# Optimization experiments

Measured on AMD Instinct MI355X. Metric: run time of the kernel, lower is better.

Reference implementation:

```python
import jax, jax.numpy as jnp
import numpy as np

INTRA_K = 16
OUTER_K = 16
MAX_PAIR = 1024


def _mahalanobis(x, cov_inv, mean):
    # x: (..., D) difference vectors; returns squared Mahalanobis-style form (...,)
    xc = x - mean
    return jnp.einsum('...i,ij,...j->...', xc, cov_inv, xc)


def setup_inputs() -> dict:
    key = jax.random.key(0)
    k1, k2, k3 = jax.random.split(key, 3)
    B, N, M = 4, 1024, 1024
    outputs = jax.random.normal(k1, (B, N, 9), dtype=jnp.float32)
    targets = jax.random.normal(k2, (B, M, 9), dtype=jnp.float32)
    mask = jax.random.randint(k3, (B, M), 0, 2).astype(bool)
    return {"outputs": outputs, "targets": targets, "mask": mask}


def reference(outputs, targets, mask):
    y_pred = outputs[:, :MAX_PAIR]                      # (B, N, 9)
    m = mask.astype(y_pred.dtype)                       # (B, M)
    cnt = m.sum()

    # mean / covariance over masked true grasps (equivalent to boolean-gather)
    mean = (targets * m[..., None]).sum((0, 1)) / cnt   # (9,)
    centered = (targets - mean) * m[..., None]          # masked rows contribute 0
    flat = centered.reshape(-1, 9)
    cov = flat.T @ flat / (cnt - 1.0)                   # (9, 9)
    cov_inv = jnp.linalg.pinv(cov)

    # intra loss: true-vs-pred pairwise distances, masked rows excluded
    diff = targets[:, :, None, :] - y_pred[:, None, :, :]   # (B, M, N, 9)
    d = _mahalanobis(diff, cov_inv, mean)                   # (B, M, N)
    neg_topk, _ = jax.lax.top_k(-d, INTRA_K)                # k smallest
    row_sum = (-neg_topk).sum(-1)                           # (B, M)
    intra_loss = (row_sum * m).sum() / cnt                  # mean over masked rows

    # outer loss: pred-vs-pred pairwise distances, no mask
    diff_r = y_pred[:, None, :, :] - y_pred[:, :, None, :]  # (B, N, N, 9); [b,i,j] = pred[b,j]-pred[b,i]
    d_r = _mahalanobis(diff_r, cov_inv, mean)               # (B, N, N)
    neg_tk, _ = jax.lax.top_k(-d_r, OUTER_K)
    outer_loss = (-neg_tk).mean()

    return intra_loss, intra_loss, outer_loss
```

## Files before the change

### kernel.cpp

```cpp
#include <hip/hip_runtime.h>
#include <math.h>

#define BB   4
#define MM   1024
#define NN   1024
#define DD   9
#define KSEL 16
#define NROW (BB * MM)
#define NSLOT (2 * NROW)
#define NBLK (NSLOT / 4)

struct Ws {
  float yT[BB * DD * NN];
  float qy[BB * NN];
  float rowsum[NSLOT];
  float part[16][55];
  float cnt;
  float mean[DD];
  float cinv[DD * DD];
};

__global__ __launch_bounds__(256) void stats_kernel(
    const float* __restrict__ targets, const int* __restrict__ mask,
    Ws* __restrict__ ws) {
  const int tid = threadIdx.x;
  const int r = blockIdx.x * 256 + tid;

  float acc[55];
#pragma unroll
  for (int k = 0; k < 55; ++k) acc[k] = 0.f;
  if (mask[r] != 0) {
    float t[DD];
#pragma unroll
    for (int k = 0; k < DD; ++k) t[k] = targets[r * DD + k];
    acc[0] = 1.f;
#pragma unroll
    for (int k = 0; k < DD; ++k) acc[1 + k] = t[k];
    int u = 10;
#pragma unroll
    for (int p = 0; p < DD; ++p)
#pragma unroll
      for (int q = p; q < DD; ++q) acc[u++] = t[p] * t[q];
  }

  __shared__ float lds[4][55];
#pragma unroll
  for (int k = 0; k < 55; ++k) {
    float v = acc[k];
#pragma unroll
    for (int off = 32; off > 0; off >>= 1) v += __shfl_down(v, off, 64);
    if ((tid & 63) == 0) lds[tid >> 6][k] = v;
  }
  __syncthreads();
  if (tid < 55)
    ws->part[blockIdx.x][tid] =
        lds[0][tid] + lds[1][tid] + lds[2][tid] + lds[3][tid];
}

__global__ __launch_bounds__(256) void prep_kernel(
    const float* __restrict__ outputs, Ws* __restrict__ ws) {
  const int tid = threadIdx.x;
  __shared__ double Sd[55];
  __shared__ float Cs[DD * DD];

  if (tid < 55) {
    double s = 0.0;
#pragma unroll
    for (int b = 0; b < 16; ++b) s += (double)ws->part[b][tid];
    Sd[tid] = s;
  }
  __syncthreads();

  if (tid < 64) {
    const int lane = tid;
    const double cnt = Sd[0];
    const int p = (lane < DD) ? lane : 0;
    double row[2 * DD];
    {
      const double mu_p = Sd[1 + p] / cnt;
#pragma unroll
      for (int q = 0; q < DD; ++q) {
        const int pp = (p < q) ? p : q;
        const int qq = (p < q) ? q : p;
        const int idx = 10 + 9 * pp - (pp * (pp - 1)) / 2 + (qq - pp);
        row[q] = (Sd[idx] - cnt * mu_p * (Sd[1 + q] / cnt)) / (cnt - 1.0);
        row[DD + q] = (p == q) ? 1.0 : 0.0;
      }
    }
#pragma unroll
    for (int c = 0; c < DD; ++c) {
      const double diag = __shfl(row[c], c, 64);
      const double dinv = 1.0 / diag;
      if (lane == c) {
#pragma unroll
        for (int q = 0; q < 2 * DD; ++q) row[q] *= dinv;
      }
      const double f = (lane == c) ? 0.0 : row[c];
#pragma unroll
      for (int q = 0; q < 2 * DD; ++q) {
        const double pv = __shfl(row[q], c, 64);
        row[q] -= f * pv;
      }
    }
    if (lane < DD) {
#pragma unroll
      for (int q = 0; q < DD; ++q) {
        const float cf = (float)row[DD + q];
        Cs[lane * DD + q] = cf;
        if (blockIdx.x == 0) ws->cinv[lane * DD + q] = cf;
      }
    }
    if (lane == 0 && blockIdx.x == 0) {
      ws->cnt = (float)cnt;
#pragma unroll
      for (int q = 0; q < DD; ++q) ws->mean[q] = (float)(Sd[1 + q] / cnt);
    }
  }
  __syncthreads();

  const int j = blockIdx.x * 256 + tid;
  const int b = j >> 10;
  const int jj = j & (NN - 1);
  float C[DD * DD];
#pragma unroll
  for (int k = 0; k < DD * DD; ++k) C[k] = Cs[k];
  float y[DD];
#pragma unroll
  for (int k = 0; k < DD; ++k) y[k] = outputs[j * DD + k];
  float q = 0.f;
#pragma unroll
  for (int p = 0; p < DD; ++p) {
    float s = 0.f;
#pragma unroll
    for (int t = 0; t < DD; ++t) s += C[p * DD + t] * y[t];
    q += y[p] * s;
    ws->yT[(b * DD + p) * NN + jj] = y[p];
  }
  ws->qy[j] = q;
}

__global__ __launch_bounds__(256) void dist_kernel(
    const float* __restrict__ outputs, const float* __restrict__ targets,
    const int* __restrict__ mask, Ws* __restrict__ ws) {
  const int wv = threadIdx.x >> 6;
  const int lane = threadIdx.x & 63;
  const int s = blockIdx.x * 4 + wv;
  const bool is_intra = (s < NROW);
  const int r = s & (NROW - 1);
  const int b = r >> 10;

  if (is_intra && mask[r] == 0) {
    if (lane == 0) ws->rowsum[s] = 0.f;
    return;
  }

  float a[DD];
  if (is_intra) {
#pragma unroll
    for (int k = 0; k < DD; ++k) a[k] = targets[r * DD + k] - ws->mean[k];
  } else {
#pragma unroll
    for (int k = 0; k < DD; ++k) a[k] = outputs[r * DD + k] + ws->mean[k];
  }
  float w[DD];
  float qa = 0.f;
#pragma unroll
  for (int p = 0; p < DD; ++p) {
    float acc = 0.f;
#pragma unroll
    for (int t = 0; t < DD; ++t) acc += ws->cinv[p * DD + t] * a[t];
    w[p] = acc;
    qa += a[p] * acc;
  }

  float v[16];
#pragma unroll
  for (int k = 0; k < 16; ++k) v[k] = 0.f;
  const float* __restrict__ yTb = ws->yT + (size_t)b * DD * NN;
#pragma unroll
  for (int p = 0; p < DD; ++p) {
    const float4* __restrict__ pl = (const float4*)(yTb + (size_t)p * NN);
#pragma unroll
    for (int c = 0; c < 4; ++c) {
      const float4 y4 = pl[c * 64 + lane];
      v[c * 4 + 0] += w[p] * y4.x;
      v[c * 4 + 1] += w[p] * y4.y;
      v[c * 4 + 2] += w[p] * y4.z;
      v[c * 4 + 3] += w[p] * y4.w;
    }
  }
  {
    const float4* __restrict__ q4 = (const float4*)(ws->qy + (size_t)b * NN);
#pragma unroll
    for (int c = 0; c < 4; ++c) {
      const float4 qv = q4[c * 64 + lane];
      v[c * 4 + 0] = qa + qv.x - 2.f * v[c * 4 + 0];
      v[c * 4 + 1] = qa + qv.y - 2.f * v[c * 4 + 1];
      v[c * 4 + 2] = qa + qv.z - 2.f * v[c * 4 + 2];
      v[c * 4 + 3] = qa + qv.w - 2.f * v[c * 4 + 3];
    }
  }

#pragma unroll
  for (int k = 2; k <= 16; k <<= 1) {
#pragma unroll
    for (int j = k >> 1; j > 0; j >>= 1) {
#pragma unroll
      for (int i = 0; i < 16; ++i) {
        const int l = i ^ j;
        if (l > i) {
          const bool up = ((i & k) == 0);
          const float lo = fminf(v[i], v[l]);
          const float hi = fmaxf(v[i], v[l]);
          v[i] = up ? lo : hi;
          v[l] = up ? hi : lo;
        }
      }
    }
  }

#pragma unroll
  for (int off = 1; off < 64; off <<= 1) {
    float pr[16];
#pragma unroll
    for (int i = 0; i < 16; ++i) pr[i] = __shfl_xor(v[i], off, 64);
#pragma unroll
    for (int i = 0; i < 16; ++i) v[i] = fminf(v[i], pr[15 - i]);
    if (off < 32) {
#pragma unroll
      for (int j = 8; j > 0; j >>= 1) {
#pragma unroll
        for (int i = 0; i < 16; ++i) {
          const int l = i ^ j;
          if (l > i) {
            const float lo = fminf(v[i], v[l]);
            const float hi = fmaxf(v[i], v[l]);
            v[i] = lo;
            v[l] = hi;
          }
        }
      }
    }
  }

  float total = v[0];
#pragma unroll
  for (int k = 1; k < 16; ++k) total += v[k];
  if (lane == 0) ws->rowsum[s] = total;
}

__global__ __launch_bounds__(256) void finalize_kernel(
    const Ws* __restrict__ ws, float* __restrict__ out) {
  const int tid = threadIdx.x;
  double li = 0.0, lo = 0.0;
  for (int k = tid; k < NROW; k += 256) {
    li += (double)ws->rowsum[k];
    lo += (double)ws->rowsum[NROW + k];
  }
#pragma unroll
  for (int off = 32; off > 0; off >>= 1) {
    li += __shfl_down(li, off, 64);
    lo += __shfl_down(lo, off, 64);
  }
  __shared__ double lds_i[4], lds_o[4];
  if ((tid & 63) == 0) {
    lds_i[tid >> 6] = li;
    lds_o[tid >> 6] = lo;
  }
  __syncthreads();
  if (tid == 0) {
    const double si = lds_i[0] + lds_i[1] + lds_i[2] + lds_i[3];
    const double so = lds_o[0] + lds_o[1] + lds_o[2] + lds_o[3];
    const float intra = (float)(si / (double)ws->cnt);
    const float outer = (float)(so / (double)(NROW * KSEL));
    out[0] = intra;
    out[1] = intra;
    out[2] = outer;
  }
}

extern "C" void kernel_launch(void* const* d_in, const int* in_sizes, int n_in,
                              void* d_out, int out_size, void* d_ws,
                              size_t ws_size, hipStream_t stream) {
  const float* outputs = (const float*)d_in[0];
  const float* targets = (const float*)d_in[1];
  const int* mask = (const int*)d_in[2];
  Ws* ws = (Ws*)d_ws;
  float* out = (float*)d_out;

  stats_kernel<<<NROW / 256, 256, 0, stream>>>(targets, mask, ws);
  prep_kernel<<<(BB * NN) / 256, 256, 0, stream>>>(outputs, ws);
  dist_kernel<<<NBLK, 256, 0, stream>>>(outputs, targets, mask, ws);
  finalize_kernel<<<1, 256, 0, stream>>>(ws, out);
}
```

Before: 97.61 us.

## Fuse stats/prep into one block and merge intra/outer rows with last-block finalize

Stats and prep are merged into a single 512-thread block, with each thread handling 8 rows and vectorized stores. The intra and outer rows for the same index now share one wave, so each yT load feeds both accumulations. Finalization runs in the last block to arrive, chosen by an atomic ticket, which removes two kernel launches. The costs are a serial single-block setup phase and more registers per wave in the distance kernel.

```diff
diff --git a/kernel.cpp b/kernel.cpp
--- a/kernel.cpp
+++ b/kernel.cpp
@@ -8,65 +8,66 @@
 #define KSEL 16
 #define NROW (BB * MM)
 #define NSLOT (2 * NROW)
-#define NBLK (NSLOT / 4)
 
 struct Ws {
   float yT[BB * DD * NN];
   float qy[BB * NN];
   float rowsum[NSLOT];
-  float part[16][55];
   float cnt;
   float mean[DD];
   float cinv[DD * DD];
+  unsigned int ticket;
 };
 
-__global__ __launch_bounds__(256) void stats_kernel(
-    const float* __restrict__ targets, const int* __restrict__ mask,
-    Ws* __restrict__ ws) {
+__global__ __launch_bounds__(512) void setup_kernel(
+    const float* __restrict__ outputs, const float* __restrict__ targets,
+    const int* __restrict__ mask, Ws* __restrict__ ws) {
   const int tid = threadIdx.x;
-  const int r = blockIdx.x * 256 + tid;
+  __shared__ float part[8][55];
+  __shared__ double Sd[55];
+  __shared__ float Cs[DD * DD];
 
   float acc[55];
 #pragma unroll
   for (int k = 0; k < 55; ++k) acc[k] = 0.f;
-  if (mask[r] != 0) {
-    float t[DD];
-#pragma unroll
-    for (int k = 0; k < DD; ++k) t[k] = targets[r * DD + k];
-    acc[0] = 1.f;
-#pragma unroll
-    for (int k = 0; k < DD; ++k) acc[1 + k] = t[k];
-    int u = 10;
-#pragma unroll
-    for (int p = 0; p < DD; ++p)
-#pragma unroll
-      for (int q = p; q < DD; ++q) acc[u++] = t[p] * t[q];
-  }
-
-  __shared__ float lds[4][55];
+  {
+    const float4* tp = (const float4*)targets + 18 * tid;
+    float4 st4[18];
+#pragma unroll
+    for (int i = 0; i < 18; ++i) st4[i] = tp[i];
+    const float* f = (const float*)st4;
+    const int4 m0 = ((const int4*)mask)[2 * tid];
+    const int4 m1 = ((const int4*)mask)[2 * tid + 1];
+    const int mk[8] = {m0.x, m0.y, m0.z, m0.w, m1.x, m1.y, m1.z, m1.w};
+#pragma unroll
+    for (int rr = 0; rr < 8; ++rr) {
+      if (mk[rr] != 0) {
+        const float* t = f + rr * DD;
+        acc[0] += 1.f;
+#pragma unroll
+        for (int k = 0; k < DD; ++k) acc[1 + k] += t[k];
+        int u = 10;
+#pragma unroll
+        for (int p = 0; p < DD; ++p)
+#pragma unroll
+          for (int q = p; q < DD; ++q) acc[u++] += t[p] * t[q];
+      }
+    }
+  }
 #pragma unroll
   for (int k = 0; k < 55; ++k) {
     float v = acc[k];
 #pragma unroll
     for (int off = 32; off > 0; off >>= 1) v += __shfl_down(v, off, 64);
-    if ((tid & 63) == 0) lds[tid >> 6][k] = v;
-  }
-  __syncthreads();
-  if (tid < 55)
-    ws->part[blockIdx.x][tid] =
-        lds[0][tid] + lds[1][tid] + lds[2][tid] + lds[3][tid];
-}
-
-__global__ __launch_bounds__(256) void prep_kernel(
-    const float* __restrict__ outputs, Ws* __restrict__ ws) {
-  const int tid = threadIdx.x;
-  __shared__ double Sd[55];
-  __shared__ float Cs[DD * DD];
+    if ((tid & 63) == 0) part[tid >> 6][k] = v;
+  }
+  if (tid == 0) ws->ticket = 0u;
+  __syncthreads();
 
   if (tid < 55) {
     double s = 0.0;
 #pragma unroll
-    for (int b = 0; b < 16; ++b) s += (double)ws->part[b][tid];
+    for (int w = 0; w < 8; ++w) s += (double)part[w][tid];
     Sd[tid] = s;
   }
   __syncthreads();
@@ -107,10 +108,10 @@
       for (int q = 0; q < DD; ++q) {
         const float cf = (float)row[DD + q];
         Cs[lane * DD + q] = cf;
-        if (blockIdx.x == 0) ws->cinv[lane * DD + q] = cf;
-      }
-    }
-    if (lane == 0 && blockIdx.x == 0) {
+        ws->cinv[lane * DD + q] = cf;
+      }
+    }
+    if (lane == 0) {
       ws->cnt = (float)cnt;
 #pragma unroll
       for (int q = 0; q < DD; ++q) ws->mean[q] = (float)(Sd[1 + q] / cnt);
@@ -118,89 +119,50 @@
   }
   __syncthreads();
 
-  const int j = blockIdx.x * 256 + tid;
-  const int b = j >> 10;
-  const int jj = j & (NN - 1);
-  float C[DD * DD];
-#pragma unroll
-  for (int k = 0; k < DD * DD; ++k) C[k] = Cs[k];
-  float y[DD];
-#pragma unroll
-  for (int k = 0; k < DD; ++k) y[k] = outputs[j * DD + k];
-  float q = 0.f;
-#pragma unroll
-  for (int p = 0; p < DD; ++p) {
-    float s = 0.f;
-#pragma unroll
-    for (int t = 0; t < DD; ++t) s += C[p * DD + t] * y[t];
-    q += y[p] * s;
-    ws->yT[(b * DD + p) * NN + jj] = y[p];
-  }
-  ws->qy[j] = q;
+  {
+    const int j0 = tid * 8;
+    const int b = j0 >> 10;
+    const int jj = j0 & (NN - 1);
+    float C[DD * DD];
+#pragma unroll
+    for (int k = 0; k < DD * DD; ++k) C[k] = Cs[k];
+    const float4* op4 = (const float4*)outputs + 18 * tid;
+    float4 so4[18];
+#pragma unroll
+    for (int i = 0; i < 18; ++i) so4[i] = op4[i];
+    const float* f = (const float*)so4;
+#pragma unroll
+    for (int g = 0; g < 2; ++g) {
+      float qv[4];
+#pragma unroll
+      for (int rr = 0; rr < 4; ++rr) {
+        const float* y = f + (g * 4 + rr) * DD;
+        float qq = 0.f;
+#pragma unroll
+        for (int p = 0; p < DD; ++p) {
+          float s = 0.f;
+#pragma unroll
+          for (int t = 0; t < DD; ++t) s += C[p * DD + t] * y[t];
+          qq += y[p] * s;
+        }
+        qv[rr] = qq;
+      }
+#pragma unroll
+      for (int p = 0; p < DD; ++p) {
+        float4 o;
+        o.x = f[(g * 4 + 0) * DD + p];
+        o.y = f[(g * 4 + 1) * DD + p];
+        o.z = f[(g * 4 + 2) * DD + p];
+        o.w = f[(g * 4 + 3) * DD + p];
+        *(float4*)(&ws->yT[(b * DD + p) * NN + jj + g * 4]) = o;
+      }
+      *(float4*)(&ws->qy[b * NN + jj + g * 4]) =
+          make_float4(qv[0], qv[1], qv[2], qv[3]);
+    }
+  }
 }
 
-__global__ __launch_bounds__(256) void dist_kernel(
-    const float* __restrict__ outputs, const float* __restrict__ targets,
-    const int* __restrict__ mask, Ws* __restrict__ ws) {
-  const int wv = threadIdx.x >> 6;
-  const int lane = threadIdx.x & 63;
-  const int s = blockIdx.x * 4 + wv;
-  const bool is_intra = (s < NROW);
-  const int r = s & (NROW - 1);
-  const int b = r >> 10;
-
-  if (is_intra && mask[r] == 0) {
-    if (lane == 0) ws->rowsum[s] = 0.f;
-    return;
-  }
-
-  float a[DD];
-  if (is_intra) {
-#pragma unroll
-    for (int k = 0; k < DD; ++k) a[k] = targets[r * DD + k] - ws->mean[k];
-  } else {
-#pragma unroll
-    for (int k = 0; k < DD; ++k) a[k] = outputs[r * DD + k] + ws->mean[k];
-  }
-  float w[DD];
-  float qa = 0.f;
-#pragma unroll
-  for (int p = 0; p < DD; ++p) {
-    float acc = 0.f;
-#pragma unroll
-    for (int t = 0; t < DD; ++t) acc += ws->cinv[p * DD + t] * a[t];
-    w[p] = acc;
-    qa += a[p] * acc;
-  }
-
-  float v[16];
-#pragma unroll
-  for (int k = 0; k < 16; ++k) v[k] = 0.f;
-  const float* __restrict__ yTb = ws->yT + (size_t)b * DD * NN;
-#pragma unroll
-  for (int p = 0; p < DD; ++p) {
-    const float4* __restrict__ pl = (const float4*)(yTb + (size_t)p * NN);
-#pragma unroll
-    for (int c = 0; c < 4; ++c) {
-      const float4 y4 = pl[c * 64 + lane];
-      v[c * 4 + 0] += w[p] * y4.x;
-      v[c * 4 + 1] += w[p] * y4.y;
-      v[c * 4 + 2] += w[p] * y4.z;
-      v[c * 4 + 3] += w[p] * y4.w;
-    }
-  }
-  {
-    const float4* __restrict__ q4 = (const float4*)(ws->qy + (size_t)b * NN);
-#pragma unroll
-    for (int c = 0; c < 4; ++c) {
-      const float4 qv = q4[c * 64 + lane];
-      v[c * 4 + 0] = qa + qv.x - 2.f * v[c * 4 + 0];
-      v[c * 4 + 1] = qa + qv.y - 2.f * v[c * 4 + 1];
-      v[c * 4 + 2] = qa + qv.z - 2.f * v[c * 4 + 2];
-      v[c * 4 + 3] = qa + qv.w - 2.f * v[c * 4 + 3];
-    }
-  }
-
+__device__ __forceinline__ float top16_sum(float (&v)[16]) {
 #pragma unroll
   for (int k = 2; k <= 16; k <<= 1) {
 #pragma unroll
@@ -218,7 +180,6 @@
       }
     }
   }
-
 #pragma unroll
   for (int off = 1; off < 64; off <<= 1) {
     float pr[16];
@@ -242,40 +203,152 @@
       }
     }
   }
-
   float total = v[0];
 #pragma unroll
   for (int k = 1; k < 16; ++k) total += v[k];
-  if (lane == 0) ws->rowsum[s] = total;
+  return total;
 }
 
-__global__ __launch_bounds__(256) void finalize_kernel(
-    const Ws* __restrict__ ws, float* __restrict__ out) {
+__global__ __launch_bounds__(256, 4) void dist_kernel(
+    const float* __restrict__ outputs, const float* __restrict__ targets,
+    const int* __restrict__ mask, Ws* __restrict__ ws,
+    float* __restrict__ out) {
   const int tid = threadIdx.x;
-  double li = 0.0, lo = 0.0;
-  for (int k = tid; k < NROW; k += 256) {
-    li += (double)ws->rowsum[k];
-    lo += (double)ws->rowsum[NROW + k];
-  }
-#pragma unroll
-  for (int off = 32; off > 0; off >>= 1) {
-    li += __shfl_down(li, off, 64);
-    lo += __shfl_down(lo, off, 64);
-  }
-  __shared__ double lds_i[4], lds_o[4];
-  if ((tid & 63) == 0) {
-    lds_i[tid >> 6] = li;
-    lds_o[tid >> 6] = lo;
-  }
-  __syncthreads();
+  const int wv = tid >> 6;
+  const int lane = tid & 63;
+  const int r = blockIdx.x * 4 + wv;
+  const int b = r >> 10;
+  const bool live = (mask[r] != 0);
+
+  float ao[DD], wo[DD];
+  float qa_o = 0.f;
+#pragma unroll
+  for (int k = 0; k < DD; ++k) ao[k] = outputs[r * DD + k] + ws->mean[k];
+#pragma unroll
+  for (int p = 0; p < DD; ++p) {
+    float s = 0.f;
+#pragma unroll
+    for (int t = 0; t < DD; ++t) s += ws->cinv[p * DD + t] * ao[t];
+    wo[p] = s;
+    qa_o += ao[p] * s;
+  }
+  float ai[DD], wi[DD];
+  float qa_i = 0.f;
+  if (live) {
+#pragma unroll
+    for (int k = 0; k < DD; ++k) ai[k] = targets[r * DD + k] - ws->mean[k];
+#pragma unroll
+    for (int p = 0; p < DD; ++p) {
+      float s = 0.f;
+#pragma unroll
+      for (int t = 0; t < DD; ++t) s += ws->cinv[p * DD + t] * ai[t];
+      wi[p] = s;
+      qa_i += ai[p] * s;
+    }
+  }
+
+  float vi[16], vo[16];
+#pragma unroll
+  for (int k = 0; k < 16; ++k) {
+    vi[k] = 0.f;
+    vo[k] = 0.f;
+  }
+  const float* __restrict__ yTb = ws->yT + (size_t)b * DD * NN;
+  if (live) {
+#pragma unroll
+    for (int p = 0; p < DD; ++p) {
+      const float4* __restrict__ pl = (const float4*)(yTb + (size_t)p * NN);
+#pragma unroll
+      for (int c = 0; c < 4; ++c) {
+        const float4 y4 = pl[c * 64 + lane];
+        vi[c * 4 + 0] += wi[p] * y4.x;
+        vi[c * 4 + 1] += wi[p] * y4.y;
+        vi[c * 4 + 2] += wi[p] * y4.z;
+        vi[c * 4 + 3] += wi[p] * y4.w;
+        vo[c * 4 + 0] += wo[p] * y4.x;
+        vo[c * 4 + 1] += wo[p] * y4.y;
+        vo[c * 4 + 2] += wo[p] * y4.z;
+        vo[c * 4 + 3] += wo[p] * y4.w;
+      }
+    }
+  } else {
+#pragma unroll
+    for (int p = 0; p < DD; ++p) {
+      const float4* __restrict__ pl = (const float4*)(yTb + (size_t)p * NN);
+#pragma unroll
+      for (int c = 0; c < 4; ++c) {
+        const float4 y4 = pl[c * 64 + lane];
+        vo[c * 4 + 0] += wo[p] * y4.x;
+        vo[c * 4 + 1] += wo[p] * y4.y;
+        vo[c * 4 + 2] += wo[p] * y4.z;
+        vo[c * 4 + 3] += wo[p] * y4.w;
+      }
+    }
+  }
+  {
+    const float4* __restrict__ q4 = (const float4*)(ws->qy + (size_t)b * NN);
+#pragma unroll
+    for (int c = 0; c < 4; ++c) {
+      const float4 qv = q4[c * 64 + lane];
+      vo[c * 4 + 0] = qa_o + qv.x - 2.f * vo[c * 4 + 0];
+      vo[c * 4 + 1] = qa_o + qv.y - 2.f * vo[c * 4 + 1];
+      vo[c * 4 + 2] = qa_o + qv.z - 2.f * vo[c * 4 + 2];
+      vo[c * 4 + 3] = qa_o + qv.w - 2.f * vo[c * 4 + 3];
+      if (live) {
+        vi[c * 4 + 0] = qa_i + qv.x - 2.f * vi[c * 4 + 0];
+        vi[c * 4 + 1] = qa_i + qv.y - 2.f * vi[c * 4 + 1];
+        vi[c * 4 + 2] = qa_i + qv.z - 2.f * vi[c * 4 + 2];
+        vi[c * 4 + 3] = qa_i + qv.w - 2.f * vi[c * 4 + 3];
+      }
+    }
+  }
+
+  float si = 0.f;
+  if (live) si = top16_sum(vi);
+  const float so = top16_sum(vo);
+  if (lane == 0) {
+    __hip_atomic_store(&ws->rowsum[r], si, __ATOMIC_RELAXED,
+                       __HIP_MEMORY_SCOPE_AGENT);
+    __hip_atomic_store(&ws->rowsum[NROW + r], so, __ATOMIC_RELAXED,
+                       __HIP_MEMORY_SCOPE_AGENT);
+  }
+
+  __syncthreads();
+  __shared__ int slast;
   if (tid == 0) {
-    const double si = lds_i[0] + lds_i[1] + lds_i[2] + lds_i[3];
-    const double so = lds_o[0] + lds_o[1] + lds_o[2] + lds_o[3];
-    const float intra = (float)(si / (double)ws->cnt);
-    const float outer = (float)(so / (double)(NROW * KSEL));
-    out[0] = intra;
-    out[1] = intra;
-    out[2] = outer;
+    const unsigned int old = __hip_atomic_fetch_add(
+        &ws->ticket, 1u, __ATOMIC_ACQ_REL, __HIP_MEMORY_SCOPE_AGENT);
+    slast = (old == (unsigned int)(gridDim.x - 1)) ? 1 : 0;
+  }
+  __syncthreads();
+  if (slast != 0) {
+    double li = 0.0, lo = 0.0;
+    for (int k = tid; k < NROW; k += 256) {
+      li += (double)__hip_atomic_load(&ws->rowsum[k], __ATOMIC_RELAXED,
+                                      __HIP_MEMORY_SCOPE_AGENT);
+      lo += (double)__hip_atomic_load(&ws->rowsum[NROW + k], __ATOMIC_RELAXED,
+                                      __HIP_MEMORY_SCOPE_AGENT);
+    }
+#pragma unroll
+    for (int off = 32; off > 0; off >>= 1) {
+      li += __shfl_down(li, off, 64);
+      lo += __shfl_down(lo, off, 64);
+    }
+    __shared__ double lds_i[4], lds_o[4];
+    if ((tid & 63) == 0) {
+      lds_i[tid >> 6] = li;
+      lds_o[tid >> 6] = lo;
+    }
+    __syncthreads();
+    if (tid == 0) {
+      const double sI = lds_i[0] + lds_i[1] + lds_i[2] + lds_i[3];
+      const double sO = lds_o[0] + lds_o[1] + lds_o[2] + lds_o[3];
+      const float intra = (float)(sI / (double)ws->cnt);
+      const float outer = (float)(sO / (double)(NROW * KSEL));
+      out[0] = intra;
+      out[1] = intra;
+      out[2] = outer;
+    }
   }
 }
 
@@ -288,8 +361,6 @@
   Ws* ws = (Ws*)d_ws;
   float* out = (float*)d_out;
 
-  stats_kernel<<<NROW / 256, 256, 0, stream>>>(targets, mask, ws);
-  prep_kernel<<<(BB * NN) / 256, 256, 0, stream>>>(outputs, ws);
-  dist_kernel<<<NBLK, 256, 0, stream>>>(outputs, targets, mask, ws);
-  finalize_kernel<<<1, 256, 0, stream>>>(ws, out);
+  setup_kernel<<<1, 512, 0, stream>>>(outputs, targets, mask, ws);
+  dist_kernel<<<NROW / 4, 256, 0, stream>>>(outputs, targets, mask, ws, out);
 }
```

Measured after the change: 125.4 us. 1.28x slower.

## Fuse stats reduction into prep kernel by redundantly computing statistics per block

Applied to the files above, without the earlier changes.

Merges the stats and prep kernels into one launch of 8 blocks of 512 threads. Each block redundantly reads all targets and mask entries, with each thread accumulating 8 rows via vectorized loads, and reduces the 55 moments in shared memory. This removes one kernel launch and the global partial-sum round trip. In exchange every block repeats the full statistics pass and the prep phase runs on only 8 blocks.

```diff
diff --git a/kernel.cpp b/kernel.cpp
--- a/kernel.cpp
+++ b/kernel.cpp
@@ -14,59 +14,66 @@
   float yT[BB * DD * NN];
   float qy[BB * NN];
   float rowsum[NSLOT];
-  float part[16][55];
   float cnt;
   float mean[DD];
   float cinv[DD * DD];
 };
 
-__global__ __launch_bounds__(256) void stats_kernel(
-    const float* __restrict__ targets, const int* __restrict__ mask,
-    Ws* __restrict__ ws) {
+__global__ __launch_bounds__(512) void prep_kernel(
+    const float* __restrict__ outputs, const float* __restrict__ targets,
+    const int* __restrict__ mask, Ws* __restrict__ ws) {
   const int tid = threadIdx.x;
-  const int r = blockIdx.x * 256 + tid;
+  __shared__ float part[8][55];
+  __shared__ double Sd[55];
+  __shared__ float Cs[DD * DD];
+
+  float4 st4[18];
+  {
+    const float4* tp = (const float4*)targets + 18 * tid;
+#pragma unroll
+    for (int i = 0; i < 18; ++i) st4[i] = tp[i];
+  }
+  const int4 m0 = ((const int4*)mask)[2 * tid];
+  const int4 m1 = ((const int4*)mask)[2 * tid + 1];
+  const int j3 = (blockIdx.x << 9) + tid;
+  float y[DD];
+#pragma unroll
+  for (int k = 0; k < DD; ++k) y[k] = outputs[j3 * DD + k];
 
   float acc[55];
 #pragma unroll
   for (int k = 0; k < 55; ++k) acc[k] = 0.f;
-  if (mask[r] != 0) {
-    float t[DD];
-#pragma unroll
-    for (int k = 0; k < DD; ++k) t[k] = targets[r * DD + k];
-    acc[0] = 1.f;
-#pragma unroll
-    for (int k = 0; k < DD; ++k) acc[1 + k] = t[k];
-    int u = 10;
-#pragma unroll
-    for (int p = 0; p < DD; ++p)
-#pragma unroll
-      for (int q = p; q < DD; ++q) acc[u++] = t[p] * t[q];
-  }
-
-  __shared__ float lds[4][55];
+  {
+    const float* f = (const float*)st4;
+    const int mk[8] = {m0.x, m0.y, m0.z, m0.w, m1.x, m1.y, m1.z, m1.w};
+#pragma unroll
+    for (int rr = 0; rr < 8; ++rr) {
+      if (mk[rr] != 0) {
+        const float* t = f + rr * DD;
+        acc[0] += 1.f;
+#pragma unroll
+        for (int k = 0; k < DD; ++k) acc[1 + k] += t[k];
+        int u = 10;
+#pragma unroll
+        for (int p = 0; p < DD; ++p)
+#pragma unroll
+          for (int q = p; q < DD; ++q) acc[u++] += t[p] * t[q];
+      }
+    }
+  }
 #pragma unroll
   for (int k = 0; k < 55; ++k) {
     float v = acc[k];
 #pragma unroll
     for (int off = 32; off > 0; off >>= 1) v += __shfl_down(v, off, 64);
-    if ((tid & 63) == 0) lds[tid >> 6][k] = v;
-  }
-  __syncthreads();
-  if (tid < 55)
-    ws->part[blockIdx.x][tid] =
-        lds[0][tid] + lds[1][tid] + lds[2][tid] + lds[3][tid];
-}
-
-__global__ __launch_bounds__(256) void prep_kernel(
-    const float* __restrict__ outputs, Ws* __restrict__ ws) {
-  const int tid = threadIdx.x;
-  __shared__ double Sd[55];
-  __shared__ float Cs[DD * DD];
+    if ((tid & 63) == 0) part[tid >> 6][k] = v;
+  }
+  __syncthreads();
 
   if (tid < 55) {
     double s = 0.0;
 #pragma unroll
-    for (int b = 0; b < 16; ++b) s += (double)ws->part[b][tid];
+    for (int w = 0; w < 8; ++w) s += (double)part[w][tid];
     Sd[tid] = s;
   }
   __syncthreads();
@@ -118,25 +125,23 @@
   }
   __syncthreads();
 
-  const int j = blockIdx.x * 256 + tid;
-  const int b = j >> 10;
-  const int jj = j & (NN - 1);
-  float C[DD * DD];
-#pragma unroll
-  for (int k = 0; k < DD * DD; ++k) C[k] = Cs[k];
-  float y[DD];
-#pragma unroll
-  for (int k = 0; k < DD; ++k) y[k] = outputs[j * DD + k];
-  float q = 0.f;
-#pragma unroll
-  for (int p = 0; p < DD; ++p) {
-    float s = 0.f;
-#pragma unroll
-    for (int t = 0; t < DD; ++t) s += C[p * DD + t] * y[t];
-    q += y[p] * s;
-    ws->yT[(b * DD + p) * NN + jj] = y[p];
-  }
-  ws->qy[j] = q;
+  {
+    const int b = j3 >> 10;
+    const int jj = j3 & (NN - 1);
+    float C[DD * DD];
+#pragma unroll
+    for (int k = 0; k < DD * DD; ++k) C[k] = Cs[k];
+    float q = 0.f;
+#pragma unroll
+    for (int p = 0; p < DD; ++p) {
+      float s = 0.f;
+#pragma unroll
+      for (int t = 0; t < DD; ++t) s += C[p * DD + t] * y[t];
+      q += y[p] * s;
+      ws->yT[(b * DD + p) * NN + jj] = y[p];
+    }
+    ws->qy[j3] = q;
+  }
 }
 
 __global__ __launch_bounds__(256) void dist_kernel(
@@ -288,8 +293,7 @@
   Ws* ws = (Ws*)d_ws;
   float* out = (float*)d_out;
 
-  stats_kernel<<<NROW / 256, 256, 0, stream>>>(targets, mask, ws);
-  prep_kernel<<<(BB * NN) / 256, 256, 0, stream>>>(outputs, ws);
+  prep_kernel<<<8, 512, 0, stream>>>(outputs, targets, mask, ws);
   dist_kernel<<<NBLK, 256, 0, stream>>>(outputs, targets, mask, ws);
   finalize_kernel<<<1, 256, 0, stream>>>(ws, out);
 }
```

Result: no change. 98.71 us (+1.1%).
